# Kernel tuning notes

Hardware: AMD Instinct MI355X
Metric: run time of the kernel (lower is better)

## Reference

```python
import jax, jax.numpy as jnp
import numpy as np

LN_EPS = 1e-5
N_HEADS = 8

def _ln(x, g, b):
    mu = jnp.mean(x, axis=-1, keepdims=True)
    var = jnp.var(x, axis=-1, keepdims=True)
    return (x - mu) * jax.lax.rsqrt(var + LN_EPS) * g + b

def _glu(x):
    a, b = jnp.split(x, 2, axis=-1)
    return a * jax.nn.sigmoid(b)

def setup_inputs() -> dict:
    key = jax.random.key(0)
    ks = iter(jax.random.split(key, 48))
    B, C, HW, p = 16, 3, 224, 16
    d, N, M = 512, 2048, 25
    Sa, So, O, T = 512, 1024, 1000, 16
    P = (HW // p) ** 2
    rn = lambda shape, s=1.0: jax.random.normal(next(ks), shape, jnp.float32) * s
    inp = {
        'x': rn((B, C, HW, HW)),
        'conv_w': rn((d, C, p, p), 0.02), 'conv_b': jnp.zeros((d,)),
        'patch_ln_g': jnp.ones((d,)), 'patch_ln_b': jnp.zeros((d,)),
        'pos': rn((1, P, d), 0.02),
        'kv_w': rn((d, d), d ** -0.5), 'kv_b': jnp.zeros((d,)),
        'kv_ln_g': jnp.ones((d,)), 'kv_ln_b': jnp.zeros((d,)),
        'q_w': rn((d, Sa), Sa ** -0.5), 'q_b': jnp.zeros((d,)),
        'attn_in_w': rn((3 * d, d), d ** -0.5), 'attn_in_b': jnp.zeros((3 * d,)),
        'attn_out_w': rn((d, d), d ** -0.5), 'attn_out_b': jnp.zeros((d,)),
        'syn_w': rn((2 * N, d + N), (d + N) ** -0.5), 'syn_b': jnp.zeros((2 * N,)),
        'syn_ln_g': jnp.ones((N,)), 'syn_ln_b': jnp.zeros((N,)),
        'fc1_w': rn((N, M, 256), (2.0 / M) ** 0.5), 'fc1_b': jnp.zeros((N, 256)),
        'fc2_w': rn((N, 128, 2), (2.0 / 128) ** 0.5), 'fc2_b': jnp.zeros((N, 2)),
        'nlm_T': jnp.ones((1,)),
        'start_state': rn((N,), (1.0 / N) ** 0.5),
        'start_trace': rn((N, M), (1.0 / (N + M)) ** 0.5),
        'decay_action': jnp.zeros((Sa,)), 'decay_out': jnp.zeros((So,)),
        'out_w': rn((O, So), So ** -0.5), 'out_b': jnp.zeros((O,)),
        'act_left': jax.random.randint(next(ks), (Sa,), 0, N, jnp.int32),
        'act_right': jax.random.randint(next(ks), (Sa,), 0, N, jnp.int32),
        'out_left': jax.random.randint(next(ks), (So,), 0, N, jnp.int32),
        'out_right': jax.random.randint(next(ks), (So,), 0, N, jnp.int32),
        'ticks': T,
    }
    return inp

def _forward(x, conv_w, conv_b, patch_ln_g, patch_ln_b, pos, kv_w, kv_b, kv_ln_g, kv_ln_b,
             q_w, q_b, attn_in_w, attn_in_b, attn_out_w, attn_out_b,
             syn_w, syn_b, syn_ln_g, syn_ln_b, fc1_w, fc1_b, fc2_w, fc2_b, nlm_T,
             start_state, start_trace, decay_action, decay_out, out_w, out_b,
             act_left, act_right, out_left, out_right, ticks):
    B = x.shape[0]
    d = conv_w.shape[0]
    hd = d // N_HEADS
    scale = 1.0 / (hd ** 0.5)
    # --- patch embedding: Conv2d(stride=patch) -> flatten -> LN, then +pos ---
    pt = jax.lax.conv_general_dilated(
        x, conv_w, (conv_w.shape[2], conv_w.shape[3]), 'VALID',
        dimension_numbers=('NCHW', 'OIHW', 'NCHW')) + conv_b[None, :, None, None]
    pt = pt.reshape(B, d, -1).transpose(0, 2, 1)            # (B, P, d)
    pt = _ln(pt, patch_ln_g, patch_ln_b) + pos
    kv = _ln(pt @ kv_w.T + kv_b, kv_ln_g, kv_ln_b)          # (B, P, d)
    wq, wk, wv = jnp.split(attn_in_w, 3)
    bq, bk, bv = jnp.split(attn_in_b, 3)
    k = (kv @ wk.T + bk).reshape(B, -1, N_HEADS, hd)        # (B, P, H, hd)
    v = (kv @ wv.T + bv).reshape(B, -1, N_HEADS, hd)
    r_a = jnp.exp(-decay_action)
    r_o = jnp.exp(-decay_out)

    def sync(act, alpha, beta, r, left, right):
        pair = act[:, left] * act[:, right]                 # (B, S)
        alpha = r * alpha + pair
        beta = r * beta + 1.0
        return alpha * jax.lax.rsqrt(beta), alpha, beta

    def nlm(trace):
        h1 = _glu(jnp.einsum('bnm,nmh->bnh', trace, fc1_w) + fc1_b)  # (B, N, 128)
        h2 = _glu(jnp.einsum('bnh,nho->bno', h1, fc2_w) + fc2_b)     # (B, N, 1)
        return h2[..., 0] / nlm_T[0]

    act0 = jnp.broadcast_to(start_state, (B,) + start_state.shape)
    trace0 = jnp.broadcast_to(start_trace, (B,) + start_trace.shape)
    Sa = act_left.shape[0]
    So = out_left.shape[0]
    _, ao0, bo0 = sync(act0, jnp.zeros((B, So)), jnp.zeros((B, So)), r_o, out_left, out_right)
    carry0 = (trace0, act0, jnp.zeros((B, Sa)), jnp.zeros((B, Sa)), ao0, bo0)

    def step(carry, _):
        trace, act, aa, ba, ao, bo = carry
        s_act, aa, ba = sync(act, aa, ba, r_a, act_left, act_right)
        qv = s_act @ q_w.T + q_b                            # (B, d)
        qh = (qv @ wq.T + bq).reshape(B, N_HEADS, hd) * scale
        attn_w = jax.nn.softmax(jnp.einsum('bhd,bphd->bhp', qh, k), axis=-1)
        attn = jnp.einsum('bhp,bphd->bhd', attn_w, v).reshape(B, d) @ attn_out_w.T + attn_out_b
        pre = jnp.concatenate([attn, act], axis=-1)         # (B, d+N)
        state = _ln(_glu(pre @ syn_w.T + syn_b), syn_ln_g, syn_ln_b)  # (B, N)
        trace = jnp.concatenate([trace[:, :, 1:], state[:, :, None]], axis=-1)
        act = nlm(trace)
        s_out, ao, bo = sync(act, ao, bo, r_o, out_left, out_right)
        pred = s_out @ out_w.T + out_b                      # (B, out_dims)
        return (trace, act, aa, ba, ao, bo), pred

    _, preds = jax.lax.scan(step, carry0, None, length=ticks)
    preds = jnp.moveaxis(preds, 0, -1)                      # (B, out_dims, ticks)
    probs = jax.nn.softmax(preds, axis=1)
    ent = -jnp.sum(probs * jnp.log(probs + 1e-10), axis=1) / jnp.log(float(preds.shape[1]))
    return preds, ent

def reference(x, conv_w, conv_b, patch_ln_g, patch_ln_b, pos, kv_w, kv_b, kv_ln_g, kv_ln_b,
              q_w, q_b, attn_in_w, attn_in_b, attn_out_w, attn_out_b,
              syn_w, syn_b, syn_ln_g, syn_ln_b, fc1_w, fc1_b, fc2_w, fc2_b, nlm_T,
              start_state, start_trace, decay_action, decay_out, out_w, out_b,
              act_left, act_right, out_left, out_right, ticks):
    return _forward(x, conv_w, conv_b, patch_ln_g, patch_ln_b, pos, kv_w, kv_b, kv_ln_g, kv_ln_b,
                    q_w, q_b, attn_in_w, attn_in_b, attn_out_w, attn_out_b,
                    syn_w, syn_b, syn_ln_g, syn_ln_b, fc1_w, fc1_b, fc2_w, fc2_b, nlm_T,
                    start_state, start_trace, decay_action, decay_out, out_w, out_b,
                    act_left, act_right, out_left, out_right, ticks)
```

## Files before the change

### kernel.cpp

```cpp
#include <hip/hip_runtime.h>
#include <hip/hip_bf16.h>
#include <math.h>


#define DEV __device__ __forceinline__
typedef const float* fp;
typedef const float4* f4p;

#define B_   16
#define P_   196
#define D_   512
#define H_   8
#define HD_  64
#define N_   2048
#define M_   25
#define SA_  512
#define SO_  1024
#define O_   1000
#define T_   16

DEV float sigmf(float x){ return 1.0f / (1.0f + expf(-x)); }
DEV float wred(float v) { for (int m = 32; m; m >>= 1) v += __shfl_xor(v, m); return v; }
DEV float f4dot(float4 a, float4 b) { return a.x*b.x + a.y*b.y + a.z*b.z + a.w*b.w; }

DEV float breduce_sum(float v, float* red) {
  int t = threadIdx.x;
  red[t] = v; __syncthreads();
  for (int s = 128; s > 0; s >>= 1) {
    if (t < s) red[t] += red[t + s];
    __syncthreads();
  }
  float r = red[0]; __syncthreads();
  return r;
}
DEV float breduce_max(float v, float* red) {
  int t = threadIdx.x;
  red[t] = v; __syncthreads();
  for (int s = 128; s > 0; s >>= 1) {
    if (t < s) red[t] = fmaxf(red[t], red[t + s]);
    __syncthreads();
  }
  float r = red[0]; __syncthreads();
  return r;
}

__global__ __launch_bounds__(256) void k_patch_tile(fp x, fp conv_w, fp conv_b, float* pt) {
  int i0 = blockIdx.x * 64;
  int j0 = blockIdx.y * 64;
  int tid = threadIdx.x;
  int ti = tid >> 4, tj = tid & 15;
  __shared__ float As[64][17];
  __shared__ float Bs[64][17];
  float acc[4][4] = {{0,0,0,0},{0,0,0,0},{0,0,0,0},{0,0,0,0}};
  int p_loc = tid >> 2, k4 = (tid & 3) * 4;
  int bp = i0 + p_loc;
  int b = bp / P_, p = bp % P_;
  int ph = p / 14, pw = p % 14;
  const float* xbase = x + (size_t)b*3*224*224 + (size_t)(ph*16)*224 + pw*16;
  for (int kc = 0; kc < 48; kc++) {
    int ci = kc >> 4, qi = kc & 15;
    float4 av = *(f4p)(xbase + ((size_t)ci*224 + qi)*224 + k4);
    As[p_loc][k4+0] = av.x; As[p_loc][k4+1] = av.y;
    As[p_loc][k4+2] = av.z; As[p_loc][k4+3] = av.w;
    float4 bv = *(f4p)(conv_w + (size_t)(j0 + p_loc)*768 + kc*16 + k4);
    Bs[p_loc][k4+0] = bv.x; Bs[p_loc][k4+1] = bv.y;
    Bs[p_loc][k4+2] = bv.z; Bs[p_loc][k4+3] = bv.w;
    __syncthreads();
    for (int kk = 0; kk < 16; kk++) {
      float a0 = As[ti*4+0][kk], a1 = As[ti*4+1][kk];
      float a2 = As[ti*4+2][kk], a3 = As[ti*4+3][kk];
      float b0 = Bs[tj*4+0][kk], b1 = Bs[tj*4+1][kk];
      float b2 = Bs[tj*4+2][kk], b3 = Bs[tj*4+3][kk];
      acc[0][0] += a0*b0; acc[0][1] += a0*b1; acc[0][2] += a0*b2; acc[0][3] += a0*b3;
      acc[1][0] += a1*b0; acc[1][1] += a1*b1; acc[1][2] += a1*b2; acc[1][3] += a1*b3;
      acc[2][0] += a2*b0; acc[2][1] += a2*b1; acc[2][2] += a2*b2; acc[2][3] += a2*b3;
      acc[3][0] += a3*b0; acc[3][1] += a3*b1; acc[3][2] += a3*b2; acc[3][3] += a3*b3;
    }
    __syncthreads();
  }
  for (int ii = 0; ii < 4; ii++)
    for (int jj = 0; jj < 4; jj++)
      pt[(size_t)(i0 + ti*4 + ii)*D_ + j0 + tj*4 + jj] = acc[ii][jj] + conv_b[j0 + tj*4 + jj];
}

__global__ __launch_bounds__(256) void k_pln(float* pt, fp g, fp bb, fp pos) {
  int bp0 = blockIdx.x * 16;
  int tid = threadIdx.x, wave = tid >> 6, lane = tid & 63;
  for (int i = 0; i < 4; i++) {
    int bp = bp0 + wave*4 + i;
    int p = bp % P_;
    float* row = pt + (size_t)bp*D_;
    float4 v0 = *(f4p)(row + lane*8);
    float4 v1 = *(f4p)(row + lane*8 + 4);
    float s = v0.x+v0.y+v0.z+v0.w + v1.x+v1.y+v1.z+v1.w;
    float q = f4dot(v0,v0) + f4dot(v1,v1);
    s = wred(s); q = wred(q);
    float mu = s / (float)D_;
    float var = q / (float)D_ - mu*mu;
    float rstd = 1.f / sqrtf(var + 1e-5f);
    for (int j = 0; j < 8; j++) {
      int c = lane*8 + j;
      float v = (j < 4) ? ((const float*)&v0)[j] : ((const float*)&v1)[j-4];
      row[c] = (v - mu)*rstd*g[c] + bb[c] + pos[p*D_ + c];
    }
  }
}

__global__ __launch_bounds__(256) void k_kv_tile(const float* ptin, fp kv_w, fp kv_b, float* kvraw) {
  int i0 = blockIdx.x * 64;
  int j0 = blockIdx.y * 64;
  int tid = threadIdx.x;
  int ti = tid >> 4, tj = tid & 15;
  __shared__ float As[64][17];
  __shared__ float Bs[64][17];
  float acc[4][4] = {{0,0,0,0},{0,0,0,0},{0,0,0,0},{0,0,0,0}};
  int p_loc = tid >> 2, k4 = (tid & 3) * 4;
  for (int kc = 0; kc < 32; kc++) {
    float4 av = *(f4p)(ptin + (size_t)(i0 + p_loc)*D_ + kc*16 + k4);
    As[p_loc][k4+0] = av.x; As[p_loc][k4+1] = av.y;
    As[p_loc][k4+2] = av.z; As[p_loc][k4+3] = av.w;
    float4 bv = *(f4p)(kv_w + (size_t)(j0 + p_loc)*D_ + kc*16 + k4);
    Bs[p_loc][k4+0] = bv.x; Bs[p_loc][k4+1] = bv.y;
    Bs[p_loc][k4+2] = bv.z; Bs[p_loc][k4+3] = bv.w;
    __syncthreads();
    for (int kk = 0; kk < 16; kk++) {
      float a0 = As[ti*4+0][kk], a1 = As[ti*4+1][kk];
      float a2 = As[ti*4+2][kk], a3 = As[ti*4+3][kk];
      float b0 = Bs[tj*4+0][kk], b1 = Bs[tj*4+1][kk];
      float b2 = Bs[tj*4+2][kk], b3 = Bs[tj*4+3][kk];
      acc[0][0] += a0*b0; acc[0][1] += a0*b1; acc[0][2] += a0*b2; acc[0][3] += a0*b3;
      acc[1][0] += a1*b0; acc[1][1] += a1*b1; acc[1][2] += a1*b2; acc[1][3] += a1*b3;
      acc[2][0] += a2*b0; acc[2][1] += a2*b1; acc[2][2] += a2*b2; acc[2][3] += a2*b3;
      acc[3][0] += a3*b0; acc[3][1] += a3*b1; acc[3][2] += a3*b2; acc[3][3] += a3*b3;
    }
    __syncthreads();
  }
  for (int ii = 0; ii < 4; ii++)
    for (int jj = 0; jj < 4; jj++)
      kvraw[(size_t)(i0 + ti*4 + ii)*D_ + j0 + tj*4 + jj] = acc[ii][jj] + kv_b[j0 + tj*4 + jj];
}

__global__ __launch_bounds__(256) void k_kvln(float* kv, fp g, fp bb) {
  int bp0 = blockIdx.x * 16;
  int tid = threadIdx.x, wave = tid >> 6, lane = tid & 63;
  for (int i = 0; i < 4; i++) {
    int bp = bp0 + wave*4 + i;
    float* row = kv + (size_t)bp*D_;
    float4 v0 = *(f4p)(row + lane*8);
    float4 v1 = *(f4p)(row + lane*8 + 4);
    float s = v0.x+v0.y+v0.z+v0.w + v1.x+v1.y+v1.z+v1.w;
    float q = f4dot(v0,v0) + f4dot(v1,v1);
    s = wred(s); q = wred(q);
    float mu = s / (float)D_;
    float var = q / (float)D_ - mu*mu;
    float rstd = 1.f / sqrtf(var + 1e-5f);
    for (int j = 0; j < 8; j++) {
      int c = lane*8 + j;
      float v = (j < 4) ? ((const float*)&v0)[j] : ((const float*)&v1)[j-4];
      row[c] = (v - mu)*rstd*g[c] + bb[c];
    }
  }
}

__global__ __launch_bounds__(256) void k_wqc(fp aw, fp q_w, float* W_qc) {
  int i0 = blockIdx.x * 16, s0 = blockIdx.y * 16;
  int tid = threadIdx.x, il = tid >> 4, sl = tid & 15;
  __shared__ float s_wq[16][129];
  __shared__ float s_qw[128][17];
  float acc = 0.f;
  for (int kc = 0; kc < 4; kc++) {
    int k0 = kc * 128;
    for (int idx = tid; idx < 2048; idx += 256) {
      int r = idx >> 7, c = idx & 127;
      s_wq[r][c] = aw[(size_t)(i0 + r)*512 + k0 + c];
    }
    for (int idx = tid; idx < 2048; idx += 256) {
      int r = idx >> 4, c = idx & 15;
      s_qw[r][c] = q_w[(size_t)(k0 + r)*512 + s0 + c];
    }
    __syncthreads();
    for (int kk = 0; kk < 128; kk++)
      acc += s_wq[il][kk] * s_qw[kk][sl];
    __syncthreads();
  }
  W_qc[(size_t)(i0 + il)*512 + s0 + sl] = 0.125f * acc;
}

__global__ __launch_bounds__(256) void k_wqcb(fp aw, fp q_b, fp ab, float* bc) {
  int i = blockIdx.x * 256 + threadIdx.x;
  float acc = ab[i];
  for (int j = 0; j < 512; j++) acc += aw[(size_t)i*512 + j] * q_b[j];
  bc[i] = 0.125f * acc;
}

__global__ void k_init(fp start_state, fp start_trace, const int* oL, const int* oR,
                       fp decay_a, fp decay_o,
                       float* act, float* trace, float* aaA, float* baA,
                       float* aoA, float* boA, float* r_a, float* r_o) {
  int gid = blockIdx.x * 256 + threadIdx.x;
  if (gid < B_*N_*M_) {
    int bn = gid / M_, m = gid % M_;
    int n = bn % N_;
    trace[gid] = start_trace[n*M_ + m];
  }
  if (gid < B_*N_) act[gid] = start_state[gid & (N_-1)];
  if (gid < B_*SA_) { aaA[gid] = 0.f; baA[gid] = 0.f; }
  if (gid < B_*SO_) {
    int s = gid & (SO_-1);
    aoA[gid] = start_state[oL[s]] * start_state[oR[s]];
    boA[gid] = 1.0f;
  }
  if (gid < SA_) r_a[gid] = expf(-decay_a[gid]);
  if (gid < SO_) r_o[gid] = expf(-decay_o[gid]);
}

__global__ __launch_bounds__(256) void k_attout(
    const float* act,
    float* aaA, float* aaB, float* baA, float* baB,
    float* aoA, float* aoB, float* boA, float* boB,
    const float* r_a, const float* r_o,
    const float* W_qc, const float* bc, const float* kvb,
    fp aw, fp ab, fp out_w, fp out_b,
    const int* aL, const int* aR, const int* oL, const int* oR,
    float* av_ws, float* out, int t) {
  __shared__ float smem[8448];
  int bid = blockIdx.x;
  int tid = threadIdx.x, wave = tid >> 6, lane = tid & 63;

  if (bid < 128) {
    const float* aaR = (t & 1) ? aaB : aaA;  float* aaW = (t & 1) ? aaA : aaB;
    const float* baR = (t & 1) ? baB : baA;  float* baW = (t & 1) ? baA : baB;
    int b = bid >> 3, h = bid & 7;
    float* sact = smem;
    float* qhh  = smem + 512;
    float* qt   = smem + 576;
    float* mW   = smem + 1088;
    float* lW   = smem + 1092;
    float* zzL  = smem + 1600;
    float* zpart= smem + 2112;
    for (int cc = 0; cc < 2; cc++) {
      int s = tid + cc*256;
      float r = r_a[s];
      float pair = act[b*N_ + aL[s]] * act[b*N_ + aR[s]];
      float a  = r*aaR[b*SA_ + s] + pair;
      float bt = r*baR[b*SA_ + s] + 1.0f;
      if (h == 0) { aaW[b*SA_ + s] = a; baW[b*SA_ + s] = bt; }
      sact[s] = a / sqrtf(bt);
    }
    __syncthreads();
    for (int k = 0; k < 16; k++) {
      int r = h*HD_ + wave*16 + k;
      const float* wr = W_qc + (size_t)r*512 + lane*4;
      float s = f4dot(*(f4p)(wr),       *(f4p)(&sact[lane*4]))
              + f4dot(*(f4p)(wr + 256), *(f4p)(&sact[lane*4 + 256]));
      s = wred(s);
      if (lane == 0) qhh[wave*16 + k] = s + bc[r];
    }
    __syncthreads();
    float acc0 = 0.f, acc1 = 0.f;
    for (int e = 0; e < HD_; e++) {
      float q = qhh[e];
      const float* ar = aw + (size_t)(512 + h*HD_ + e)*D_;
      acc0 += q * ar[tid];
      acc1 += q * ar[tid + 256];
    }
    qt[tid] = acc0; qt[tid + 256] = acc1;
    float kb = 0.f;
    for (int e = 0; e < HD_; e++) kb += qhh[e] * ab[512 + h*HD_ + e];
    __syncthreads();
    float qreg[8];
    for (int j = 0; j < 8; j++) qreg[j] = qt[lane*8 + j];
    float m = -1e30f, l = 0.f;
    float zz8[8] = {0,0,0,0,0,0,0,0};
    for (int p = wave*49; p < wave*49 + 49; p++) {
      const float* kvp = kvb + ((size_t)(b*P_ + p))*D_ + lane*8;
      float4 v0 = *(f4p)(kvp), v1 = *(f4p)(kvp + 4);
      float d = v0.x*qreg[0] + v0.y*qreg[1] + v0.z*qreg[2] + v0.w*qreg[3]
              + v1.x*qreg[4] + v1.y*qreg[5] + v1.z*qreg[6] + v1.w*qreg[7];
      d = wred(d);
      float s_p = d + kb;
      float m_new = fmaxf(m, s_p);
      float scale = expf(m - m_new);
      float e = expf(s_p - m_new);
      l = l*scale + e;
      zz8[0] = zz8[0]*scale + e*v0.x; zz8[1] = zz8[1]*scale + e*v0.y;
      zz8[2] = zz8[2]*scale + e*v0.z; zz8[3] = zz8[3]*scale + e*v0.w;
      zz8[4] = zz8[4]*scale + e*v1.x; zz8[5] = zz8[5]*scale + e*v1.y;
      zz8[6] = zz8[6]*scale + e*v1.z; zz8[7] = zz8[7]*scale + e*v1.w;
      m = m_new;
    }
    if (lane == 0) { mW[wave] = m; lW[wave] = l; }
    for (int j = 0; j < 8; j++) zpart[wave*512 + lane*8 + j] = zz8[j];
    __syncthreads();
    {
      float M0 = fmaxf(fmaxf(mW[0], mW[1]), fmaxf(mW[2], mW[3]));
      float f0 = expf(mW[0]-M0), f1 = expf(mW[1]-M0), f2 = expf(mW[2]-M0), f3 = expf(mW[3]-M0);
      float L = lW[0]*f0 + lW[1]*f1 + lW[2]*f2 + lW[3]*f3;
      float invL = 1.f / L;
      for (int cc = 0; cc < 2; cc++) {
        int c = tid + cc*256;
        zzL[c] = (zpart[c]*f0 + zpart[512 + c]*f1 + zpart[1024 + c]*f2 + zpart[1536 + c]*f3) * invL;
      }
    }
    __syncthreads();
    for (int k = 0; k < 16; k++) {
      int e2 = wave*16 + k;
      int r = 1024 + h*HD_ + e2;
      const float* wr = aw + (size_t)r*512 + lane*4;
      float s = f4dot(*(f4p)(wr),       *(f4p)(&zzL[lane*4]))
              + f4dot(*(f4p)(wr + 256), *(f4p)(&zzL[lane*4 + 256]));
      s = wred(s);
      if (lane == 0) av_ws[b*D_ + h*HD_ + e2] = s + ab[r];
    }
  } else if (t > 0) {
    int s_ = t - 1;
    const float* aoR = (s_ & 1) ? aoB : aoA;  float* aoW = (s_ & 1) ? aoA : aoB;
    const float* boR = (s_ & 1) ? boB : boA;  float* boW = (s_ & 1) ? boA : boB;
    int obid = bid - 128;
    int rb = obid >> 1, bg = obid & 1;
    float* s_sout = smem;
    for (int i = 0; i < 32; i++) {
      int idx = tid + i*256;
      int bb = idx >> 10, s = idx & 1023;
      int b = bg*8 + bb;
      float r = r_o[s];
      float pair = act[b*N_ + oL[s]] * act[b*N_ + oR[s]];
      float a  = r*aoR[b*SO_ + s] + pair;
      float bt = r*boR[b*SO_ + s] + 1.f;
      if (rb == 0) { aoW[b*SO_ + s] = a; boW[b*SO_ + s] = bt; }
      s_sout[bb*1024 + s] = a / sqrtf(bt);
    }
    __syncthreads();
    for (int k = 0; k < 5; k++) {
      int r = rb*20 + wave*5 + k;
      const float* wr = out_w + (size_t)r*1024 + lane*4;
      float4 w0 = *(f4p)(wr),       w1 = *(f4p)(wr + 256),
             w2 = *(f4p)(wr + 512), w3 = *(f4p)(wr + 768);
      float pp[8];
      for (int bb = 0; bb < 8; bb++) {
        const float* pb = &s_sout[bb*1024 + lane*4];
        pp[bb] = f4dot(w0, *(f4p)(pb))       + f4dot(w1, *(f4p)(pb + 256))
               + f4dot(w2, *(f4p)(pb + 512)) + f4dot(w3, *(f4p)(pb + 768));
      }
      float obr = out_b[r];
      for (int bb = 0; bb < 8; bb++) {
        float s = wred(pp[bb]);
        if (lane == 0) out[((size_t)((bg*8 + bb)*O_ + r))*T_ + s_] = s + obr;
      }
    }
  }
}

__global__ __launch_bounds__(256) void k_ao2(const float* av_ws, fp ow, fp ob, float* attn_o) {
  int rb = blockIdx.x, bg = blockIdx.y;
  int tid = threadIdx.x, wave = tid >> 6, lane = tid & 63;
  __shared__ float s_a[8][516];
  for (int idx = tid; idx < 8*512; idx += 256) {
    int bb = idx >> 9, c = idx & 511;
    s_a[bb][c] = av_ws[(bg*8 + bb)*D_ + c];
  }
  __syncthreads();
  for (int k = 0; k < 8; k++) {
    int r = rb*32 + wave*8 + k;
    const float* wr = ow + (size_t)r*512 + lane*4;
    float4 w0 = *(f4p)(wr), w1 = *(f4p)(wr + 256);
    float pp[8];
    for (int bb = 0; bb < 8; bb++) {
      const float* pb = &s_a[bb][lane*4];
      pp[bb] = f4dot(w0, *(f4p)(pb)) + f4dot(w1, *(f4p)(pb + 256));
    }
    float obr = ob[r];
    for (int bb = 0; bb < 8; bb++) {
      float s = wred(pp[bb]);
      if (lane == 0) attn_o[(bg*8 + bb)*D_ + r] = s + obr;
    }
  }
}

__global__ __launch_bounds__(256) void k_syn(const float* attn_o, const float* act,
                                             fp syn_w, fp syn_b, float* ysyn,
                                             float* psum, float* psq) {
  int rb = blockIdx.x, bg = blockIdx.y;
  int tid = threadIdx.x, wave = tid >> 6, lane = tid & 63;
  __shared__ float pre8[8*2560];
  __shared__ float wsum[4][8], wsq[4][8];
  for (int bb = 0; bb < 8; bb++) {
    int b = bg*8 + bb;
    for (int i = tid; i < 2560; i += 256)
      pre8[bb*2560 + i] = (i < 512) ? attn_o[b*D_ + i] : act[b*N_ + (i - 512)];
  }
  __syncthreads();
  float lsum[8] = {0,0,0,0,0,0,0,0}, lsq[8] = {0,0,0,0,0,0,0,0};
  for (int k = 0; k < 4; k++) {
    int pr = rb*16 + wave*4 + k;
    float sA[8];
    {
      const float* wr = syn_w + (size_t)pr*2560 + lane*4;
      float4 wreg[10];
      for (int j = 0; j < 10; j++) wreg[j] = *(f4p)(wr + j*256);
      float pp[8] = {0,0,0,0,0,0,0,0};
      for (int j = 0; j < 10; j++) {
        int idx = lane*4 + j*256;
        for (int bb = 0; bb < 8; bb++)
          pp[bb] += f4dot(wreg[j], *(f4p)(&pre8[bb*2560 + idx]));
      }
      float sb = syn_b[pr];
      for (int bb = 0; bb < 8; bb++) sA[bb] = wred(pp[bb]) + sb;
    }
    {
      int r2 = pr + 2048;
      const float* wr = syn_w + (size_t)r2*2560 + lane*4;
      float4 wreg[10];
      for (int j = 0; j < 10; j++) wreg[j] = *(f4p)(wr + j*256);
      float pp[8] = {0,0,0,0,0,0,0,0};
      for (int j = 0; j < 10; j++) {
        int idx = lane*4 + j*256;
        for (int bb = 0; bb < 8; bb++)
          pp[bb] += f4dot(wreg[j], *(f4p)(&pre8[bb*2560 + idx]));
      }
      float sb = syn_b[r2];
      for (int bb = 0; bb < 8; bb++) {
        float sG = wred(pp[bb]) + sb;
        float v = sA[bb] * sigmf(sG);
        lsum[bb] += v; lsq[bb] += v*v;
        if (lane == 0) ysyn[(size_t)(bg*8 + bb)*N_ + pr] = v;
      }
    }
  }
  if (lane == 0)
    for (int bb = 0; bb < 8; bb++) { wsum[wave][bb] = lsum[bb]; wsq[wave][bb] = lsq[bb]; }
  __syncthreads();
  if (tid < 8) {
    float s1 = wsum[0][tid] + wsum[1][tid] + wsum[2][tid] + wsum[3][tid];
    float s2 = wsq[0][tid]  + wsq[1][tid]  + wsq[2][tid]  + wsq[3][tid];
    psum[rb*16 + bg*8 + tid] = s1;
    psq [rb*16 + bg*8 + tid] = s2;
  }
}

__global__ __launch_bounds__(256) void k_nlm(float* trace, const float* ysyn,
                                             const float* psum, const float* psq,
                                             fp sg, fp sb2,
                                             fp fc1_w, fp fc1_b, fp fc2_w, fp fc2_b,
                                             fp nlmT, float* act) {
  int n = blockIdx.x, tid = threadIdx.x;
  __shared__ float tr[B_][M_];
  __shared__ float uu[256][17];
  __shared__ float h1[128][17];
  __shared__ float vout[B_][2];
  __shared__ float s_mu[16], s_rstd[16];
  {
    int b = tid >> 4, j = tid & 15;
    if (tid < 256) {
      float s1 = 0.f, s2 = 0.f;
      for (int rb = j; rb < 128; rb += 16) { s1 += psum[rb*16 + b]; s2 += psq[rb*16 + b]; }
      for (int m = 8; m; m >>= 1) { s1 += __shfl_xor(s1, m); s2 += __shfl_xor(s2, m); }
      if (j == 0) {
        float mu = s1 / (float)N_;
        s_mu[b] = mu;
        s_rstd[b] = 1.f / sqrtf(s2 / (float)N_ - mu*mu + 1e-5f);
      }
    }
  }
  __syncthreads();
  for (int i = tid; i < B_*M_; i += 256) {
    int b = i / M_, m = i % M_;
    float v;
    if (m < M_-1) v = trace[((size_t)(b*N_ + n))*M_ + m + 1];
    else          v = (ysyn[(size_t)b*N_ + n] - s_mu[b]) * s_rstd[b] * sg[n] + sb2[n];
    tr[b][m] = v;
  }
  __syncthreads();
  for (int i = tid; i < B_*M_; i += 256) {
    int b = i / M_, m = i % M_;
    trace[((size_t)(b*N_ + n))*M_ + m] = tr[b][m];
  }
  float w25[M_];
  for (int m = 0; m < M_; m++) w25[m] = fc1_w[((size_t)n*M_ + m)*256 + tid];
  float bias = fc1_b[n*256 + tid];
  for (int b = 0; b < B_; b++) {
    float u = bias;
    for (int m = 0; m < M_; m++) u += tr[b][m]*w25[m];
    uu[tid][b] = u;
  }
  __syncthreads();
  if (tid < 128) {
    for (int b = 0; b < B_; b++)
      h1[tid][b] = uu[tid][b] * sigmf(uu[tid + 128][b]);
  }
  __syncthreads();
  if (tid < 32) {
    int b = tid >> 1, o = tid & 1;
    float acc = fc2_b[n*2 + o];
    for (int hh = 0; hh < 128; hh++) acc += h1[hh][b] * fc2_w[((size_t)n*128 + hh)*2 + o];
    vout[b][o] = acc;
  }
  __syncthreads();
  if (tid < B_) {
    act[tid*N_ + n] = vout[tid][0] * sigmf(vout[tid][1]) / nlmT[0];
  }
}

__global__ __launch_bounds__(256) void k_out(const float* act, const float* aoR, const float* boR,
                                             float* aoW, float* boW, const float* r_o,
                                             const int* L, const int* R,
                                             fp out_w, fp out_b, float* out, int t) {
  int rb = blockIdx.x, bg = blockIdx.y;
  int tid = threadIdx.x, wave = tid >> 6, lane = tid & 63;
  __shared__ float s_sout[8][1024];
  for (int i = 0; i < 32; i++) {
    int idx = tid + i*256;
    int bb = idx >> 10, s = idx & 1023;
    int b = bg*8 + bb;
    float r = r_o[s];
    float pair = act[b*N_ + L[s]] * act[b*N_ + R[s]];
    float a  = r*aoR[b*SO_ + s] + pair;
    float bt = r*boR[b*SO_ + s] + 1.f;
    if (rb == 0) { aoW[b*SO_ + s] = a; boW[b*SO_ + s] = bt; }
    s_sout[bb][s] = a / sqrtf(bt);
  }
  __syncthreads();
  for (int k = 0; k < 5; k++) {
    int r = rb*20 + wave*5 + k;
    const float* wr = out_w + (size_t)r*1024 + lane*4;
    float4 w0 = *(f4p)(wr),       w1 = *(f4p)(wr + 256),
           w2 = *(f4p)(wr + 512), w3 = *(f4p)(wr + 768);
    float pp[8];
    for (int bb = 0; bb < 8; bb++) {
      const float* pb = &s_sout[bb][lane*4];
      pp[bb] = f4dot(w0, *(f4p)(pb))       + f4dot(w1, *(f4p)(pb + 256))
             + f4dot(w2, *(f4p)(pb + 512)) + f4dot(w3, *(f4p)(pb + 768));
    }
    float obr = out_b[r];
    for (int bb = 0; bb < 8; bb++) {
      float s = wred(pp[bb]);
      if (lane == 0) out[((size_t)((bg*8 + bb)*O_ + r))*T_ + t] = s + obr;
    }
  }
}

__global__ __launch_bounds__(256) void k_final(float* out) {
  int b = blockIdx.x, t = blockIdx.y, tid = threadIdx.x;
  __shared__ float red[256];
  float lm = -1e30f;
  for (int o = tid; o < O_; o += 256) lm = fmaxf(lm, out[((size_t)(b*O_ + o))*T_ + t]);
  float Mx = breduce_max(lm, red);
  float le = 0.f;
  for (int o = tid; o < O_; o += 256) le += expf(out[((size_t)(b*O_ + o))*T_ + t] - Mx);
  float S = breduce_sum(le, red);
  float lt = 0.f;
  for (int o = tid; o < O_; o += 256) {
    float pr = expf(out[((size_t)(b*O_ + o))*T_ + t] - Mx) / S;
    lt += pr * logf(pr + 1e-10f);
  }
  float E = breduce_sum(lt, red);
  if (tid == 0)
    out[(size_t)B_*O_*T_ + b*T_ + t] = -E / logf((float)O_);
}

extern "C" void kernel_launch(void* const* d_in, const int* in_sizes, int n_in,
                              void* d_out, int out_size, void* d_ws, size_t ws_size,
                              hipStream_t stream) {
  (void)in_sizes; (void)n_in; (void)out_size; (void)ws_size;
  fp x          = (fp)d_in[0];
  fp conv_w     = (fp)d_in[1];
  fp conv_b     = (fp)d_in[2];
  fp patch_ln_g = (fp)d_in[3];
  fp patch_ln_b = (fp)d_in[4];
  fp pos        = (fp)d_in[5];
  fp kv_w       = (fp)d_in[6];
  fp kv_b       = (fp)d_in[7];
  fp kv_ln_g    = (fp)d_in[8];
  fp kv_ln_b    = (fp)d_in[9];
  fp q_w        = (fp)d_in[10];
  fp q_b        = (fp)d_in[11];
  fp attn_in_w  = (fp)d_in[12];
  fp attn_in_b  = (fp)d_in[13];
  fp attn_out_w = (fp)d_in[14];
  fp attn_out_b = (fp)d_in[15];
  fp syn_w      = (fp)d_in[16];
  fp syn_b      = (fp)d_in[17];
  fp syn_ln_g   = (fp)d_in[18];
  fp syn_ln_b   = (fp)d_in[19];
  fp fc1_w      = (fp)d_in[20];
  fp fc1_b      = (fp)d_in[21];
  fp fc2_w      = (fp)d_in[22];
  fp fc2_b      = (fp)d_in[23];
  fp nlm_T      = (fp)d_in[24];
  fp start_state= (fp)d_in[25];
  fp start_trace= (fp)d_in[26];
  fp decay_a    = (fp)d_in[27];
  fp decay_o    = (fp)d_in[28];
  fp out_w      = (fp)d_in[29];
  fp out_b      = (fp)d_in[30];
  const int* act_left  = (const int*)d_in[31];
  const int* act_right = (const int*)d_in[32];
  const int* out_left  = (const int*)d_in[33];
  const int* out_right = (const int*)d_in[34];

  float* ws = (float*)d_ws;
  float* pt     = ws;
  float* act    = ws + 0;
  float* trace  = ws + 32768;
  float* aaA    = ws + 851968;
  float* aaB    = ws + 860160;
  float* baA    = ws + 868352;
  float* baB    = ws + 876544;
  float* aoA    = ws + 884736;
  float* aoB    = ws + 901120;
  float* boA    = ws + 917504;
  float* boB    = ws + 933888;
  float* attn_o = ws + 958464;
  float* ysyn   = ws + 966656;
  float* psum   = ws + 999424;
  float* psq    = ws + 1001472;
  float* av_ws  = ws + 1064960;
  float* r_a    = ws + 1073152;
  float* r_o    = ws + 1073664;
  float* W_qc   = ws + 1074688;
  float* bc     = ws + 1336832;
  float* kvb    = ws + 1605632;

  k_patch_tile<<<dim3(49, 8), dim3(256), 0, stream>>>(x, conv_w, conv_b, pt);
  k_pln<<<dim3(196), dim3(256), 0, stream>>>(pt, patch_ln_g, patch_ln_b, pos);
  k_kv_tile<<<dim3(49, 8), dim3(256), 0, stream>>>(pt, kv_w, kv_b, kvb);
  k_kvln<<<dim3(196), dim3(256), 0, stream>>>(kvb, kv_ln_g, kv_ln_b);
  k_wqc<<<dim3(32, 32), dim3(256), 0, stream>>>(attn_in_w, q_w, W_qc);
  k_wqcb<<<dim3(2), dim3(256), 0, stream>>>(attn_in_w, q_b, attn_in_b, bc);
  k_init<<<dim3((B_*N_*M_ + 255)/256), dim3(256), 0, stream>>>(start_state, start_trace,
        out_left, out_right, decay_a, decay_o, act, trace, aaA, baA, aoA, boA, r_a, r_o);

  for (int t = 0; t < T_; t++) {
    k_attout<<<dim3(228), dim3(256), 0, stream>>>(
        act, aaA, aaB, baA, baB, aoA, aoB, boA, boB, r_a, r_o,
        W_qc, bc, kvb, attn_in_w, attn_in_b, out_w, out_b,
        act_left, act_right, out_left, out_right, av_ws, (float*)d_out, t);
    k_ao2<<<dim3(16, 2), dim3(256), 0, stream>>>(av_ws, attn_out_w, attn_out_b, attn_o);
    k_syn<<<dim3(128, 2), dim3(256), 0, stream>>>(attn_o, act, syn_w, syn_b, ysyn, psum, psq);
    k_nlm<<<dim3(N_), dim3(256), 0, stream>>>(trace, ysyn, psum, psq, syn_ln_g, syn_ln_b,
                                              fc1_w, fc1_b, fc2_w, fc2_b, nlm_T, act);
  }
  {
    int t = T_ - 1;
    const float* aoR = (t & 1) ? aoB : aoA;  float* aoW = (t & 1) ? aoA : aoB;
    const float* boR = (t & 1) ? boB : boA;  float* boW = (t & 1) ? boA : boB;
    k_out<<<dim3(50, 2), dim3(256), 0, stream>>>(act, aoR, boR, aoW, boW, r_o,
                                                 out_left, out_right, out_w, out_b,
                                                 (float*)d_out, t);
  }
  k_final<<<dim3(16, 16), dim3(256), 0, stream>>>((float*)d_out);
}
```

Measured before the change: 2.976 ms.

## Restructure attention, synapse and output kernels to share weights across all batches

```diff
diff --git a/kernel.cpp b/kernel.cpp
--- a/kernel.cpp
+++ b/kernel.cpp
@@ -49,8 +49,8 @@
   int j0 = blockIdx.y * 64;
   int tid = threadIdx.x;
   int ti = tid >> 4, tj = tid & 15;
-  __shared__ float As[64][17];
-  __shared__ float Bs[64][17];
+  __shared__ float As[64][20];
+  __shared__ float Bs[64][20];
   float acc[4][4] = {{0,0,0,0},{0,0,0,0},{0,0,0,0},{0,0,0,0}};
   int p_loc = tid >> 2, k4 = (tid & 3) * 4;
   int bp = i0 + p_loc;
@@ -59,12 +59,8 @@
   const float* xbase = x + (size_t)b*3*224*224 + (size_t)(ph*16)*224 + pw*16;
   for (int kc = 0; kc < 48; kc++) {
     int ci = kc >> 4, qi = kc & 15;
-    float4 av = *(f4p)(xbase + ((size_t)ci*224 + qi)*224 + k4);
-    As[p_loc][k4+0] = av.x; As[p_loc][k4+1] = av.y;
-    As[p_loc][k4+2] = av.z; As[p_loc][k4+3] = av.w;
-    float4 bv = *(f4p)(conv_w + (size_t)(j0 + p_loc)*768 + kc*16 + k4);
-    Bs[p_loc][k4+0] = bv.x; Bs[p_loc][k4+1] = bv.y;
-    Bs[p_loc][k4+2] = bv.z; Bs[p_loc][k4+3] = bv.w;
+    *(float4*)&As[p_loc][k4] = *(f4p)(xbase + ((size_t)ci*224 + qi)*224 + k4);
+    *(float4*)&Bs[p_loc][k4] = *(f4p)(conv_w + (size_t)(j0 + p_loc)*768 + kc*16 + k4);
     __syncthreads();
     for (int kk = 0; kk < 16; kk++) {
       float a0 = As[ti*4+0][kk], a1 = As[ti*4+1][kk];
@@ -111,17 +107,13 @@
   int j0 = blockIdx.y * 64;
   int tid = threadIdx.x;
   int ti = tid >> 4, tj = tid & 15;
-  __shared__ float As[64][17];
-  __shared__ float Bs[64][17];
+  __shared__ float As[64][20];
+  __shared__ float Bs[64][20];
   float acc[4][4] = {{0,0,0,0},{0,0,0,0},{0,0,0,0},{0,0,0,0}};
   int p_loc = tid >> 2, k4 = (tid & 3) * 4;
   for (int kc = 0; kc < 32; kc++) {
-    float4 av = *(f4p)(ptin + (size_t)(i0 + p_loc)*D_ + kc*16 + k4);
-    As[p_loc][k4+0] = av.x; As[p_loc][k4+1] = av.y;
-    As[p_loc][k4+2] = av.z; As[p_loc][k4+3] = av.w;
-    float4 bv = *(f4p)(kv_w + (size_t)(j0 + p_loc)*D_ + kc*16 + k4);
-    Bs[p_loc][k4+0] = bv.x; Bs[p_loc][k4+1] = bv.y;
-    Bs[p_loc][k4+2] = bv.z; Bs[p_loc][k4+3] = bv.w;
+    *(float4*)&As[p_loc][k4] = *(f4p)(ptin + (size_t)(i0 + p_loc)*D_ + kc*16 + k4);
+    *(float4*)&Bs[p_loc][k4] = *(f4p)(kv_w + (size_t)(j0 + p_loc)*D_ + kc*16 + k4);
     __syncthreads();
     for (int kk = 0; kk < 16; kk++) {
       float a0 = As[ti*4+0][kk], a1 = As[ti*4+1][kk];
@@ -223,111 +215,105 @@
     fp aw, fp ab, fp out_w, fp out_b,
     const int* aL, const int* aR, const int* oL, const int* oR,
     float* av_ws, float* out, int t) {
-  __shared__ float smem[8448];
+  __shared__ float smem[16384];
   int bid = blockIdx.x;
   int tid = threadIdx.x, wave = tid >> 6, lane = tid & 63;
 
-  if (bid < 128) {
+  if (bid < 32) {
     const float* aaR = (t & 1) ? aaB : aaA;  float* aaW = (t & 1) ? aaA : aaB;
     const float* baR = (t & 1) ? baB : baA;  float* baW = (t & 1) ? baA : baB;
-    int b = bid >> 3, h = bid & 7;
+    int b = bid >> 1, half = bid & 1;
+    int h = half*4 + wave;
     float* sact = smem;
     float* qhh  = smem + 512;
-    float* qt   = smem + 576;
-    float* mW   = smem + 1088;
-    float* lW   = smem + 1092;
-    float* zzL  = smem + 1600;
-    float* zpart= smem + 2112;
+    float* zzs  = smem + 768;
+    float* skv  = smem + 2848;
     for (int cc = 0; cc < 2; cc++) {
       int s = tid + cc*256;
       float r = r_a[s];
       float pair = act[b*N_ + aL[s]] * act[b*N_ + aR[s]];
       float a  = r*aaR[b*SA_ + s] + pair;
       float bt = r*baR[b*SA_ + s] + 1.0f;
-      if (h == 0) { aaW[b*SA_ + s] = a; baW[b*SA_ + s] = bt; }
+      if (half == 0) { aaW[b*SA_ + s] = a; baW[b*SA_ + s] = bt; }
       sact[s] = a / sqrtf(bt);
     }
     __syncthreads();
-    for (int k = 0; k < 16; k++) {
-      int r = h*HD_ + wave*16 + k;
+    for (int k = 0; k < 64; k++) {
+      int r = h*HD_ + k;
       const float* wr = W_qc + (size_t)r*512 + lane*4;
       float s = f4dot(*(f4p)(wr),       *(f4p)(&sact[lane*4]))
               + f4dot(*(f4p)(wr + 256), *(f4p)(&sact[lane*4 + 256]));
       s = wred(s);
-      if (lane == 0) qhh[wave*16 + k] = s + bc[r];
-    }
-    __syncthreads();
-    float acc0 = 0.f, acc1 = 0.f;
-    for (int e = 0; e < HD_; e++) {
-      float q = qhh[e];
-      const float* ar = aw + (size_t)(512 + h*HD_ + e)*D_;
-      acc0 += q * ar[tid];
-      acc1 += q * ar[tid + 256];
-    }
-    qt[tid] = acc0; qt[tid + 256] = acc1;
-    float kb = 0.f;
-    for (int e = 0; e < HD_; e++) kb += qhh[e] * ab[512 + h*HD_ + e];
-    __syncthreads();
-    float qreg[8];
-    for (int j = 0; j < 8; j++) qreg[j] = qt[lane*8 + j];
+      if (lane == 0) qhh[wave*64 + k] = s + bc[r];
+    }
+    __syncthreads();
+    float4 q0 = {0,0,0,0}, q1 = {0,0,0,0};
+    for (int e = 0; e < 64; e++) {
+      float qv = qhh[wave*64 + e];
+      const float* ar = aw + (size_t)(512 + h*HD_ + e)*D_ + lane*8;
+      float4 a0 = *(f4p)(ar), a1 = *(f4p)(ar + 4);
+      q0.x += qv*a0.x; q0.y += qv*a0.y; q0.z += qv*a0.z; q0.w += qv*a0.w;
+      q1.x += qv*a1.x; q1.y += qv*a1.y; q1.z += qv*a1.z; q1.w += qv*a1.w;
+    }
+    float kbv = qhh[wave*64 + lane] * ab[512 + h*HD_ + lane];
+    kbv = wred(kbv);
     float m = -1e30f, l = 0.f;
-    float zz8[8] = {0,0,0,0,0,0,0,0};
-    for (int p = wave*49; p < wave*49 + 49; p++) {
-      const float* kvp = kvb + ((size_t)(b*P_ + p))*D_ + lane*8;
-      float4 v0 = *(f4p)(kvp), v1 = *(f4p)(kvp + 4);
-      float d = v0.x*qreg[0] + v0.y*qreg[1] + v0.z*qreg[2] + v0.w*qreg[3]
-              + v1.x*qreg[4] + v1.y*qreg[5] + v1.z*qreg[6] + v1.w*qreg[7];
-      d = wred(d);
-      float s_p = d + kb;
-      float m_new = fmaxf(m, s_p);
-      float scale = expf(m - m_new);
-      float e = expf(s_p - m_new);
-      l = l*scale + e;
-      zz8[0] = zz8[0]*scale + e*v0.x; zz8[1] = zz8[1]*scale + e*v0.y;
-      zz8[2] = zz8[2]*scale + e*v0.z; zz8[3] = zz8[3]*scale + e*v0.w;
-      zz8[4] = zz8[4]*scale + e*v1.x; zz8[5] = zz8[5]*scale + e*v1.y;
-      zz8[6] = zz8[6]*scale + e*v1.z; zz8[7] = zz8[7]*scale + e*v1.w;
-      m = m_new;
-    }
-    if (lane == 0) { mW[wave] = m; lW[wave] = l; }
-    for (int j = 0; j < 8; j++) zpart[wave*512 + lane*8 + j] = zz8[j];
-    __syncthreads();
-    {
-      float M0 = fmaxf(fmaxf(mW[0], mW[1]), fmaxf(mW[2], mW[3]));
-      float f0 = expf(mW[0]-M0), f1 = expf(mW[1]-M0), f2 = expf(mW[2]-M0), f3 = expf(mW[3]-M0);
-      float L = lW[0]*f0 + lW[1]*f1 + lW[2]*f2 + lW[3]*f3;
-      float invL = 1.f / L;
-      for (int cc = 0; cc < 2; cc++) {
-        int c = tid + cc*256;
-        zzL[c] = (zpart[c]*f0 + zpart[512 + c]*f1 + zpart[1024 + c]*f2 + zpart[1536 + c]*f3) * invL;
+    float4 z0 = {0,0,0,0}, z1 = {0,0,0,0};
+    for (int ch = 0; ch < 13; ch++) {
+      int p0 = ch*16;
+      int cnt = (p0 + 16 <= P_) ? 16 : (P_ - p0);
+      __syncthreads();
+      for (int i = 0; i < 8; i++) {
+        int fi = i*256 + tid;
+        int r = fi >> 7, c4 = fi & 127;
+        int gp = p0 + r; if (gp > P_-1) gp = P_-1;
+        *(float4*)&skv[r*520 + c4*4] = *(f4p)(kvb + ((size_t)(b*P_ + gp))*D_ + c4*4);
       }
-    }
-    __syncthreads();
-    for (int k = 0; k < 16; k++) {
-      int e2 = wave*16 + k;
-      int r = 1024 + h*HD_ + e2;
+      __syncthreads();
+      for (int p = 0; p < cnt; p++) {
+        const float* kp = &skv[p*520 + lane*8];
+        float4 v0 = *(f4p)(kp), v1 = *(f4p)(kp + 4);
+        float d = f4dot(v0, q0) + f4dot(v1, q1);
+        d = wred(d);
+        float s_p = d + kbv;
+        float mn = fmaxf(m, s_p);
+        float sc = expf(m - mn), e = expf(s_p - mn);
+        l = l*sc + e;
+        z0.x = z0.x*sc + e*v0.x; z0.y = z0.y*sc + e*v0.y;
+        z0.z = z0.z*sc + e*v0.z; z0.w = z0.w*sc + e*v0.w;
+        z1.x = z1.x*sc + e*v1.x; z1.y = z1.y*sc + e*v1.y;
+        z1.z = z1.z*sc + e*v1.z; z1.w = z1.w*sc + e*v1.w;
+        m = mn;
+      }
+    }
+    float invl = 1.f / l;
+    zzs[wave*520 + lane*8 + 0] = z0.x*invl; zzs[wave*520 + lane*8 + 1] = z0.y*invl;
+    zzs[wave*520 + lane*8 + 2] = z0.z*invl; zzs[wave*520 + lane*8 + 3] = z0.w*invl;
+    zzs[wave*520 + lane*8 + 4] = z1.x*invl; zzs[wave*520 + lane*8 + 5] = z1.y*invl;
+    zzs[wave*520 + lane*8 + 6] = z1.z*invl; zzs[wave*520 + lane*8 + 7] = z1.w*invl;
+    __syncthreads();
+    for (int k = 0; k < 64; k++) {
+      int r = 1024 + h*HD_ + k;
       const float* wr = aw + (size_t)r*512 + lane*4;
-      float s = f4dot(*(f4p)(wr),       *(f4p)(&zzL[lane*4]))
-              + f4dot(*(f4p)(wr + 256), *(f4p)(&zzL[lane*4 + 256]));
+      float s = f4dot(*(f4p)(wr),       *(f4p)(&zzs[wave*520 + lane*4]))
+              + f4dot(*(f4p)(wr + 256), *(f4p)(&zzs[wave*520 + 256 + lane*4]));
       s = wred(s);
-      if (lane == 0) av_ws[b*D_ + h*HD_ + e2] = s + ab[r];
+      if (lane == 0) av_ws[b*D_ + h*HD_ + k] = s + ab[r];
     }
   } else if (t > 0) {
     int s_ = t - 1;
     const float* aoR = (s_ & 1) ? aoB : aoA;  float* aoW = (s_ & 1) ? aoA : aoB;
     const float* boR = (s_ & 1) ? boB : boA;  float* boW = (s_ & 1) ? boA : boB;
-    int obid = bid - 128;
-    int rb = obid >> 1, bg = obid & 1;
+    int rb = bid - 32;
     float* s_sout = smem;
-    for (int i = 0; i < 32; i++) {
-      int idx = tid + i*256;
-      int bb = idx >> 10, s = idx & 1023;
-      int b = bg*8 + bb;
+    for (int i = 0; i < 64; i++) {
+      int e = i*256 + tid;
+      int bb = e >> 10, s = e & 1023;
       float r = r_o[s];
-      float pair = act[b*N_ + oL[s]] * act[b*N_ + oR[s]];
-      float a  = r*aoR[b*SO_ + s] + pair;
-      float bt = r*boR[b*SO_ + s] + 1.f;
-      if (rb == 0) { aoW[b*SO_ + s] = a; boW[b*SO_ + s] = bt; }
+      float pair = act[bb*N_ + oL[s]] * act[bb*N_ + oR[s]];
+      float a  = r*aoR[bb*SO_ + s] + pair;
+      float bt = r*boR[bb*SO_ + s] + 1.f;
+      if (rb == 0) { aoW[bb*SO_ + s] = a; boW[bb*SO_ + s] = bt; }
       s_sout[bb*1024 + s] = a / sqrtf(bt);
     }
     __syncthreads();
@@ -336,16 +322,16 @@
       const float* wr = out_w + (size_t)r*1024 + lane*4;
       float4 w0 = *(f4p)(wr),       w1 = *(f4p)(wr + 256),
              w2 = *(f4p)(wr + 512), w3 = *(f4p)(wr + 768);
-      float pp[8];
-      for (int bb = 0; bb < 8; bb++) {
+      float pp[16];
+      for (int bb = 0; bb < 16; bb++) {
         const float* pb = &s_sout[bb*1024 + lane*4];
         pp[bb] = f4dot(w0, *(f4p)(pb))       + f4dot(w1, *(f4p)(pb + 256))
                + f4dot(w2, *(f4p)(pb + 512)) + f4dot(w3, *(f4p)(pb + 768));
       }
       float obr = out_b[r];
-      for (int bb = 0; bb < 8; bb++) {
+      for (int bb = 0; bb < 16; bb++) {
         float s = wred(pp[bb]);
-        if (lane == 0) out[((size_t)((bg*8 + bb)*O_ + r))*T_ + s_] = s + obr;
+        if (lane == 0) out[((size_t)(bb*O_ + r))*T_ + s_] = s + obr;
       }
     }
   }
@@ -380,61 +366,52 @@
 __global__ __launch_bounds__(256) void k_syn(const float* attn_o, const float* act,
                                              fp syn_w, fp syn_b, float* ysyn,
                                              float* psum, float* psq) {
-  int rb = blockIdx.x, bg = blockIdx.y;
+  int bid = blockIdx.x;
   int tid = threadIdx.x, wave = tid >> 6, lane = tid & 63;
-  __shared__ float pre8[8*2560];
-  __shared__ float wsum[4][8], wsq[4][8];
-  for (int bb = 0; bb < 8; bb++) {
-    int b = bg*8 + bb;
-    for (int i = tid; i < 2560; i += 256)
-      pre8[bb*2560 + i] = (i < 512) ? attn_o[b*D_ + i] : act[b*N_ + (i - 512)];
-  }
-  __syncthreads();
-  float lsum[8] = {0,0,0,0,0,0,0,0}, lsq[8] = {0,0,0,0,0,0,0,0};
-  for (int k = 0; k < 4; k++) {
-    int pr = rb*16 + wave*4 + k;
-    float sA[8];
-    {
-      const float* wr = syn_w + (size_t)pr*2560 + lane*4;
-      float4 wreg[10];
-      for (int j = 0; j < 10; j++) wreg[j] = *(f4p)(wr + j*256);
-      float pp[8] = {0,0,0,0,0,0,0,0};
-      for (int j = 0; j < 10; j++) {
-        int idx = lane*4 + j*256;
-        for (int bb = 0; bb < 8; bb++)
-          pp[bb] += f4dot(wreg[j], *(f4p)(&pre8[bb*2560 + idx]));
+  __shared__ float s_pre[16][260];
+  __shared__ float wsum[4][16], wsq[4][16];
+  float accA[2][16], accG[2][16];
+  for (int k = 0; k < 2; k++)
+    for (int bb = 0; bb < 16; bb++) { accA[k][bb] = 0.f; accG[k][bb] = 0.f; }
+  int pr0 = bid*8 + wave*2;
+  for (int cc = 0; cc < 10; cc++) {
+    __syncthreads();
+    int g = cc*256 + tid;
+    for (int i = 0; i < 16; i++)
+      s_pre[i][tid] = (g < 512) ? attn_o[i*D_ + g] : act[i*N_ + (g - 512)];
+    __syncthreads();
+    for (int k = 0; k < 2; k++) {
+      int pr = pr0 + k;
+      float4 wA = *(f4p)(syn_w + (size_t)pr*2560 + cc*256 + lane*4);
+      float4 wG = *(f4p)(syn_w + (size_t)(pr + 2048)*2560 + cc*256 + lane*4);
+      for (int bb = 0; bb < 16; bb++) {
+        float4 pv = *(f4p)(&s_pre[bb][lane*4]);
+        accA[k][bb] += f4dot(wA, pv);
+        accG[k][bb] += f4dot(wG, pv);
       }
-      float sb = syn_b[pr];
-      for (int bb = 0; bb < 8; bb++) sA[bb] = wred(pp[bb]) + sb;
-    }
-    {
-      int r2 = pr + 2048;
-      const float* wr = syn_w + (size_t)r2*2560 + lane*4;
-      float4 wreg[10];
-      for (int j = 0; j < 10; j++) wreg[j] = *(f4p)(wr + j*256);
-      float pp[8] = {0,0,0,0,0,0,0,0};
-      for (int j = 0; j < 10; j++) {
-        int idx = lane*4 + j*256;
-        for (int bb = 0; bb < 8; bb++)
-          pp[bb] += f4dot(wreg[j], *(f4p)(&pre8[bb*2560 + idx]));
-      }
-      float sb = syn_b[r2];
-      for (int bb = 0; bb < 8; bb++) {
-        float sG = wred(pp[bb]) + sb;
-        float v = sA[bb] * sigmf(sG);
-        lsum[bb] += v; lsq[bb] += v*v;
-        if (lane == 0) ysyn[(size_t)(bg*8 + bb)*N_ + pr] = v;
-      }
+    }
+  }
+  float lsv[16], lqv[16];
+  for (int bb = 0; bb < 16; bb++) { lsv[bb] = 0.f; lqv[bb] = 0.f; }
+  for (int k = 0; k < 2; k++) {
+    int pr = pr0 + k;
+    float sbA = syn_b[pr], sbG = syn_b[pr + 2048];
+    for (int bb = 0; bb < 16; bb++) {
+      float a = wred(accA[k][bb]) + sbA;
+      float gg = wred(accG[k][bb]) + sbG;
+      float v = a * sigmf(gg);
+      lsv[bb] += v; lqv[bb] += v*v;
+      if (lane == 0) ysyn[(size_t)bb*N_ + pr] = v;
     }
   }
   if (lane == 0)
-    for (int bb = 0; bb < 8; bb++) { wsum[wave][bb] = lsum[bb]; wsq[wave][bb] = lsq[bb]; }
-  __syncthreads();
-  if (tid < 8) {
+    for (int bb = 0; bb < 16; bb++) { wsum[wave][bb] = lsv[bb]; wsq[wave][bb] = lqv[bb]; }
+  __syncthreads();
+  if (tid < 16) {
     float s1 = wsum[0][tid] + wsum[1][tid] + wsum[2][tid] + wsum[3][tid];
     float s2 = wsq[0][tid]  + wsq[1][tid]  + wsq[2][tid]  + wsq[3][tid];
-    psum[rb*16 + bg*8 + tid] = s1;
-    psq [rb*16 + bg*8 + tid] = s2;
+    psum[bid*16 + tid] = s1;
+    psq [bid*16 + tid] = s2;
   }
 }
 
@@ -451,15 +428,13 @@
   __shared__ float s_mu[16], s_rstd[16];
   {
     int b = tid >> 4, j = tid & 15;
-    if (tid < 256) {
-      float s1 = 0.f, s2 = 0.f;
-      for (int rb = j; rb < 128; rb += 16) { s1 += psum[rb*16 + b]; s2 += psq[rb*16 + b]; }
-      for (int m = 8; m; m >>= 1) { s1 += __shfl_xor(s1, m); s2 += __shfl_xor(s2, m); }
-      if (j == 0) {
-        float mu = s1 / (float)N_;
-        s_mu[b] = mu;
-        s_rstd[b] = 1.f / sqrtf(s2 / (float)N_ - mu*mu + 1e-5f);
-      }
+    float s1 = 0.f, s2 = 0.f;
+    for (int rb = j; rb < 256; rb += 16) { s1 += psum[rb*16 + b]; s2 += psq[rb*16 + b]; }
+    for (int m = 8; m; m >>= 1) { s1 += __shfl_xor(s1, m); s2 += __shfl_xor(s2, m); }
+    if (j == 0) {
+      float mu = s1 / (float)N_;
+      s_mu[b] = mu;
+      s_rstd[b] = 1.f / sqrtf(s2 / (float)N_ - mu*mu + 1e-5f);
     }
   }
   __syncthreads();
@@ -505,19 +480,18 @@
                                              float* aoW, float* boW, const float* r_o,
                                              const int* L, const int* R,
                                              fp out_w, fp out_b, float* out, int t) {
-  int rb = blockIdx.x, bg = blockIdx.y;
+  int rb = blockIdx.x;
   int tid = threadIdx.x, wave = tid >> 6, lane = tid & 63;
-  __shared__ float s_sout[8][1024];
-  for (int i = 0; i < 32; i++) {
-    int idx = tid + i*256;
-    int bb = idx >> 10, s = idx & 1023;
-    int b = bg*8 + bb;
+  __shared__ float s_sout[16*1024];
+  for (int i = 0; i < 64; i++) {
+    int e = i*256 + tid;
+    int bb = e >> 10, s = e & 1023;
     float r = r_o[s];
-    float pair = act[b*N_ + L[s]] * act[b*N_ + R[s]];
-    float a  = r*aoR[b*SO_ + s] + pair;
-    float bt = r*boR[b*SO_ + s] + 1.f;
-    if (rb == 0) { aoW[b*SO_ + s] = a; boW[b*SO_ + s] = bt; }
-    s_sout[bb][s] = a / sqrtf(bt);
+    float pair = act[bb*N_ + L[s]] * act[bb*N_ + R[s]];
+    float a  = r*aoR[bb*SO_ + s] + pair;
+    float bt = r*boR[bb*SO_ + s] + 1.f;
+    if (rb == 0) { aoW[bb*SO_ + s] = a; boW[bb*SO_ + s] = bt; }
+    s_sout[bb*1024 + s] = a / sqrtf(bt);
   }
   __syncthreads();
   for (int k = 0; k < 5; k++) {
@@ -525,16 +499,16 @@
     const float* wr = out_w + (size_t)r*1024 + lane*4;
     float4 w0 = *(f4p)(wr),       w1 = *(f4p)(wr + 256),
            w2 = *(f4p)(wr + 512), w3 = *(f4p)(wr + 768);
-    float pp[8];
-    for (int bb = 0; bb < 8; bb++) {
-      const float* pb = &s_sout[bb][lane*4];
+    float pp[16];
+    for (int bb = 0; bb < 16; bb++) {
+      const float* pb = &s_sout[bb*1024 + lane*4];
       pp[bb] = f4dot(w0, *(f4p)(pb))       + f4dot(w1, *(f4p)(pb + 256))
              + f4dot(w2, *(f4p)(pb + 512)) + f4dot(w3, *(f4p)(pb + 768));
     }
     float obr = out_b[r];
-    for (int bb = 0; bb < 8; bb++) {
+    for (int bb = 0; bb < 16; bb++) {
       float s = wred(pp[bb]);
-      if (lane == 0) out[((size_t)((bg*8 + bb)*O_ + r))*T_ + t] = s + obr;
+      if (lane == 0) out[((size_t)(bb*O_ + r))*T_ + t] = s + obr;
     }
   }
 }
@@ -613,7 +587,7 @@
   float* attn_o = ws + 958464;
   float* ysyn   = ws + 966656;
   float* psum   = ws + 999424;
-  float* psq    = ws + 1001472;
+  float* psq    = ws + 1003520;
   float* av_ws  = ws + 1064960;
   float* r_a    = ws + 1073152;
   float* r_o    = ws + 1073664;
@@ -631,12 +605,12 @@
         out_left, out_right, decay_a, decay_o, act, trace, aaA, baA, aoA, boA, r_a, r_o);
 
   for (int t = 0; t < T_; t++) {
-    k_attout<<<dim3(228), dim3(256), 0, stream>>>(
+    k_attout<<<dim3(82), dim3(256), 0, stream>>>(
         act, aaA, aaB, baA, baB, aoA, aoB, boA, boB, r_a, r_o,
         W_qc, bc, kvb, attn_in_w, attn_in_b, out_w, out_b,
         act_left, act_right, out_left, out_right, av_ws, (float*)d_out, t);
     k_ao2<<<dim3(16, 2), dim3(256), 0, stream>>>(av_ws, attn_out_w, attn_out_b, attn_o);
-    k_syn<<<dim3(128, 2), dim3(256), 0, stream>>>(attn_o, act, syn_w, syn_b, ysyn, psum, psq);
+    k_syn<<<dim3(256), dim3(256), 0, stream>>>(attn_o, act, syn_w, syn_b, ysyn, psum, psq);
     k_nlm<<<dim3(N_), dim3(256), 0, stream>>>(trace, ysyn, psum, psq, syn_ln_g, syn_ln_b,
                                               fc1_w, fc1_b, fc2_w, fc2_b, nlm_T, act);
   }
@@ -644,9 +618,9 @@
     int t = T_ - 1;
     const float* aoR = (t & 1) ? aoB : aoA;  float* aoW = (t & 1) ? aoA : aoB;
     const float* boR = (t & 1) ? boB : boA;  float* boW = (t & 1) ? boA : boB;
-    k_out<<<dim3(50, 2), dim3(256), 0, stream>>>(act, aoR, boR, aoW, boW, r_o,
-                                                 out_left, out_right, out_w, out_b,
-                                                 (float*)d_out, t);
+    k_out<<<dim3(50), dim3(256), 0, stream>>>(act, aoR, boR, aoW, boW, r_o,
+                                              out_left, out_right, out_w, out_b,
+                                              (float*)d_out, t);
   }
   k_final<<<dim3(16, 16), dim3(256), 0, stream>>>((float*)d_out);
 }
```

After: 4.459 ms. 49.8% more time.
